# Kernel tuning notes

Hardware: AMD Instinct MI355X
Metric: run time of the kernel (lower is better)

The kernel has to match this reference:

```python
import jax, jax.numpy as jnp
import numpy as np

K_MASK = -2.3819763e+38
B, L, D = 2, 2048, 2048
NQ, NKV, H = 8, 4, 256
Q_SCALE = 0.0625  # head_dim ** -0.5
ROPE_BASE = 10000.0
SOFT_CAP = 50.0
WINDOW = 512
EPS = 1e-6


def apply_rope(x, positions, base=ROPE_BASE):
    # x: [B, L, N, H], positions: [B, L]; rope_proportion=1.0 -> no nope pad
    head_dim = x.shape[-1]
    half = head_dim // 2
    freq_exp = 2.0 / head_dim * jnp.arange(half, dtype=jnp.float32)
    timescale = base ** freq_exp                                   # [H/2]
    ang = positions[..., None].astype(jnp.float32) / timescale     # [B, L, H/2]
    ang = ang[..., None, :]                                        # [B, L, 1, H/2]
    sin, cos = jnp.sin(ang), jnp.cos(ang)
    x1, x2 = jnp.split(x, 2, axis=-1)
    out = jnp.concatenate([x1 * cos - x2 * sin, x2 * cos + x1 * sin], axis=-1)
    return out.astype(x.dtype)


def rms_norm(x, scale, eps=EPS):
    var = jnp.mean(jnp.square(x), axis=-1, keepdims=True)
    return x * jax.lax.rsqrt(var + eps) * (1.0 + scale)


def sliding_window_mask(positions, window):
    # bidirectional window: total size `window` split left/right
    q_pos = positions[:, :, None]
    k_pos = positions[:, None, :]
    dist = q_pos - k_pos
    left = (window + 1) // 2
    right = window // 2 + 1
    return ((dist >= 0) & (dist < left)) | ((dist < 0) & (-dist < right))  # [B, L, L]


def setup_inputs() -> dict:
    key = jax.random.key(0)
    ks = jax.random.split(key, 4)
    x = jax.random.normal(ks[0], (B, L, D), dtype=jnp.float32)
    segment_pos = jnp.tile(jnp.arange(L, dtype=jnp.int32)[None, :], (B, 1))
    attn_mask = jnp.ones((B, L, L), dtype=jnp.bool_)
    q_w = 0.01 * jax.random.normal(ks[1], (NQ, D, H), dtype=jnp.float32)
    kv_w = 0.01 * jax.random.normal(ks[2], (2, NKV, D, H), dtype=jnp.float32)
    o_w = 0.01 * jax.random.normal(ks[3], (NQ, H, D), dtype=jnp.float32)
    q_scale = jnp.zeros((H,), dtype=jnp.float32)
    k_scale = jnp.zeros((H,), dtype=jnp.float32)
    return {"x": x, "segment_pos": segment_pos, "attn_mask": attn_mask,
            "q_w": q_w, "kv_w": kv_w, "o_w": o_w,
            "q_scale": q_scale, "k_scale": k_scale}


def reference(x, segment_pos, attn_mask, q_w, kv_w, o_w, q_scale, k_scale):
    # projections (GQA path: num_kv_heads != num_q_heads)
    q = jnp.einsum('BTD,NDH->BTNH', x, q_w)                   # [B,T,NQ,H]
    kv = jnp.einsum('BSD,CKDH->CBSKH', x, kv_w)
    k, v = kv[0], kv[1]                                       # [B,S,NKV,H]
    # QK-RMSNorm
    q = rms_norm(q, q_scale)
    k = rms_norm(k, k_scale)
    # RoPE + query scaling
    q = apply_rope(q, segment_pos) * Q_SCALE
    k = apply_rope(k, segment_pos)
    # grouped logits
    G = NQ // NKV
    q = q.reshape(B, L, NKV, G, H)
    logits = jnp.einsum('BTKGH,BSKH->BTKGS', q, k).reshape(B, L, NQ, L)
    # soft cap
    logits = jnp.tanh(logits / SOFT_CAP) * SOFT_CAP
    # bidirectional sliding-window mask combined with attn_mask
    mask = attn_mask & sliding_window_mask(segment_pos, WINDOW)  # [B,L,L]
    padded = jnp.where(mask[:, :, None, :], logits, K_MASK)
    probs = jax.nn.softmax(padded, axis=-1).astype(k.dtype)
    probs = probs.reshape(B, L, NKV, G, L)
    enc = jnp.einsum('BTKGS,BSKH->BTKGH', probs, v).reshape(B, L, NQ, H)
    return jnp.einsum('BTNH,NHD->BTD', enc, o_w)
```

## Files before the change

kernel.cpp:

```cpp
#include <hip/hip_runtime.h>
#include <stdint.h>

#define B_   2
#define L_   2048
#define D_   2048
#define NQh  8
#define NKVh 4
#define H_   256

typedef __attribute__((ext_vector_type(8))) short bf16x8;
typedef __attribute__((ext_vector_type(4))) float f32x4;
typedef __attribute__((ext_vector_type(4))) unsigned short u16x4;

typedef __attribute__((address_space(1))) unsigned int as1_uint;
typedef __attribute__((address_space(3))) unsigned int as3_uint;

#define MFMA16(a, b, c) __builtin_amdgcn_mfma_f32_16x16x32_bf16((a), (b), (c), 0, 0, 0)

__device__ __forceinline__ unsigned short f2b(float f) {
  uint32_t u = __builtin_bit_cast(uint32_t, f);
  u += 0x7FFFu + ((u >> 16) & 1u);
  return (unsigned short)(u >> 16);
}

__device__ __forceinline__ void gload16(const unsigned short* g, unsigned short* l) {
  __builtin_amdgcn_global_load_lds((as1_uint*)g, (as3_uint*)l, 16, 0, 0);
}

template<int N> __device__ __forceinline__ void vmwait() {
  if constexpr (N == 8)      asm volatile("s_waitcnt vmcnt(8)" ::: "memory");
  else if constexpr (N == 6) asm volatile("s_waitcnt vmcnt(6)" ::: "memory");
  else if constexpr (N == 4) asm volatile("s_waitcnt vmcnt(4)" ::: "memory");
  else if constexpr (N == 3) asm volatile("s_waitcnt vmcnt(3)" ::: "memory");
  else                       asm volatile("s_waitcnt vmcnt(0)" ::: "memory");
}

__global__ void k_cvt_x(const float* __restrict__ x, unsigned short* __restrict__ xb) {
  int i = blockIdx.x * blockDim.x + threadIdx.x;
  float4 v = ((const float4*)x)[i];
  u16x4 o;
  o.x = f2b(v.x); o.y = f2b(v.y); o.z = f2b(v.z); o.w = f2b(v.w);
  ((u16x4*)xb)[i] = o;
}

__global__ void k_build_wt(const float* __restrict__ qw, const float* __restrict__ kvw,
                           unsigned short* __restrict__ Wt) {
  __shared__ float tile[32][33];
  int hb = blockIdx.z;
  int h0 = blockIdx.y * 32, d0 = blockIdx.x * 32;
  const float* src; int rowbase;
  if (hb < 8) { src = qw + (size_t)hb * D_ * H_;       rowbase = hb * 256; }
  else        { src = kvw + (size_t)(hb - 8) * D_ * H_; rowbase = 2048 + (hb - 8) * 256; }
  int tx = threadIdx.x & 31, ty = threadIdx.x >> 5;
  for (int i = 0; i < 4; i++) {
    int d = ty + i * 8;
    tile[d][tx] = src[(size_t)(d0 + d) * H_ + h0 + tx];
  }
  __syncthreads();
  for (int i = 0; i < 4; i++) {
    int h = ty + i * 8;
    Wt[(size_t)(rowbase + h0 + h) * D_ + d0 + tx] = f2b(tile[tx][h]);
  }
}

__global__ void k_build_owt(const float* __restrict__ ow, unsigned short* __restrict__ Owt) {
  __shared__ float tile[32][33];
  int r0 = blockIdx.y * 32, d0 = blockIdx.x * 32;
  int tx = threadIdx.x & 31, ty = threadIdx.x >> 5;
  for (int i = 0; i < 4; i++) {
    int r = ty + i * 8;
    tile[r][tx] = ow[(size_t)(r0 + r) * D_ + d0 + tx];
  }
  __syncthreads();
  for (int i = 0; i < 4; i++) {
    int d = ty + i * 8;
    Owt[(size_t)(d0 + d) * 2048 + r0 + tx] = f2b(tile[tx][d]);
  }
}

__global__ __launch_bounds__(512, 2) void k_gemm64(const unsigned short* __restrict__ A,
                                                   const unsigned short* __restrict__ Bt,
                                                   float* __restrict__ C, int Ndim, int Kdim) {
  __shared__ __align__(16) unsigned short lds[65536];

  const int t = threadIdx.x;
  const int w = t >> 6, l = t & 63;
  const int wr = w >> 2, wc = w & 3;
  const int g = l >> 4, c = l & 15;
  const int m0 = blockIdx.y * 256, n0 = blockIdx.x * 256;
  const int NI = Kdim >> 7;

  const int chunk = ((l & 3) ^ ((l >> 3) & 3)) * 8;
  const unsigned short* Ag = A  + (size_t)(m0 + w * 16 + (l >> 2)) * Kdim + chunk;
  const unsigned short* Bg = Bt + (size_t)(n0 + w * 16 + (l >> 2)) * Kdim + chunk;
  const int rsw = (g ^ ((c >> 1) & 3)) * 8;

  auto stageA = [&](int kt, int ks) {
    unsigned short* dst = &lds[(kt & 1) * 32768 + ks * 8192 + w * 512];
    const unsigned short* src = Ag + (size_t)kt * 64 + ks * 32;
    gload16(src, dst);
    gload16(src + (size_t)128 * Kdim, dst + 4096);
  };
  auto stageB = [&](int kt, int ks) {
    unsigned short* dst = &lds[(kt & 1) * 32768 + 16384 + ks * 8192 + w * 512];
    const unsigned short* src = Bg + (size_t)kt * 64 + ks * 32;
    gload16(src, dst);
    gload16(src + (size_t)128 * Kdim, dst + 4096);
  };

  bf16x8 af[8];
  auto ldA = [&](int slot, int ks) {
#pragma unroll
    for (int m = 0; m < 8; m++)
      af[m] = *(const bf16x8*)&lds[slot * 32768 + ks * 8192 + (wr * 128 + m * 16 + c) * 32 + rsw];
  };
  auto ldB = [&](int slot, int ks, int n) {
    return *(const bf16x8*)&lds[slot * 32768 + 16384 + ks * 8192 + (wc * 64 + n * 16 + c) * 32 + rsw];
  };

  f32x4 acc[8][4] = {};

#define GPH(SLOT, KS, NH, DO_LDA, STAGE_STMT, VM_STMT)                        \
  {                                                                           \
    if (DO_LDA) ldA(SLOT, KS);                                                \
    bf16x8 b0 = ldB(SLOT, KS, (NH) * 2);                                      \
    bf16x8 b1 = ldB(SLOT, KS, (NH) * 2 + 1);                                  \
    STAGE_STMT;                                                               \
    __builtin_amdgcn_s_barrier();                                             \
    asm volatile("s_waitcnt lgkmcnt(0)" ::: "memory");                        \
    __builtin_amdgcn_s_setprio(1);                                            \
    _Pragma("unroll")                                                         \
    for (int m = 0; m < 8; m++) {                                             \
      acc[m][(NH) * 2]     = MFMA16(af[m], b0, acc[m][(NH) * 2]);             \
      acc[m][(NH) * 2 + 1] = MFMA16(af[m], b1, acc[m][(NH) * 2 + 1]);         \
    }                                                                         \
    __builtin_amdgcn_s_setprio(0);                                            \
    VM_STMT;                                                                  \
    __builtin_amdgcn_s_barrier();                                             \
  }

  stageA(0, 0); stageB(0, 0);
  stageA(0, 1); stageB(0, 1);
  stageA(1, 0); stageB(1, 0);
  vmwait<8>();
  __builtin_amdgcn_s_barrier();

  for (int i = 0; i < NI; i++) {
    const int ta = 2 * i, tb = 2 * i + 1;
    const bool nl = (i + 1 < NI);
    GPH(0, 0, 0, true,  { stageA(tb, 1); }, {});
    GPH(0, 0, 1, false, { stageB(tb, 1); }, { vmwait<8>(); });
    GPH(0, 1, 0, true,  { if (nl) stageA(ta + 2, 0); }, {});
    GPH(0, 1, 1, false, { if (nl) stageB(ta + 2, 0); },
        { if (nl) vmwait<8>(); else vmwait<4>(); });
    GPH(1, 0, 0, true,  { if (nl) stageA(ta + 2, 1); }, {});
    GPH(1, 0, 1, false, { if (nl) stageB(ta + 2, 1); },
        { if (nl) vmwait<8>(); else vmwait<0>(); });
    GPH(1, 1, 0, true,  { if (nl) stageA(tb + 2, 0); }, {});
    GPH(1, 1, 1, false, { if (nl) stageB(tb + 2, 0); }, { if (nl) vmwait<8>(); });
  }
#undef GPH

#pragma unroll
  for (int m = 0; m < 8; m++)
#pragma unroll
    for (int n = 0; n < 4; n++) {
      int row = m0 + wr * 128 + m * 16 + g * 4;
      int col = n0 + wc * 64 + n * 16 + c;
      float* cp = &C[(size_t)row * Ndim + col];
#pragma unroll
      for (int r = 0; r < 4; r++) cp[(size_t)r * Ndim] = acc[m][n][r];
    }
}

template<int BM, int BN>
__global__ __launch_bounds__(512, 2) void k_gemm8p(const unsigned short* __restrict__ A,
                                                   const unsigned short* __restrict__ Bt,
                                                   float* __restrict__ C, int Ndim, int Kdim) {
  constexpr int MF  = BM / 32;
  constexpr int NF  = 4;
  constexpr int ASZ = BM * 32, BSZ = BN * 32;
  constexpr int SLOT = ASZ + BSZ;
  constexpr int LA  = BM / 128, LB = BN / 128;
  constexpr int U   = LA + LB;
  constexpr int NPH = (MF * NF) / 16;
  __shared__ __align__(16) unsigned short lds[4 * SLOT];

  const int t = threadIdx.x;
  const int w = t >> 6, l = t & 63;
  const int wr = w >> 2, wc = w & 3;
  const int g = l >> 4, c = l & 15;
  const int m0 = blockIdx.y * BM, n0 = blockIdx.x * BN;
  const int NT = Kdim >> 5;

  const int kswz = ((l & 3) ^ ((l >> 3) & 3)) * 8;
  const unsigned short* Ag = A  + (size_t)(m0 + w * 16 + (l >> 2)) * Kdim + kswz;
  const unsigned short* Bg = Bt + (size_t)(n0 + w * 16 + (l >> 2)) * Kdim + kswz;
  const int ldsA = w * 512;
  const int ldsB = ASZ + w * 512;
  const int gsw = (g ^ ((c >> 1) & 3)) * 8;

  auto stageA = [&](int kt) {
    int s = kt & 3;
#pragma unroll
    for (int j = 0; j < LA; j++)
      gload16(Ag + (size_t)j * 128 * Kdim + kt * 32, &lds[s * SLOT + ldsA + j * 4096]);
  };
  auto stageB = [&](int kt) {
    int s = kt & 3;
#pragma unroll
    for (int j = 0; j < LB; j++)
      gload16(Bg + (size_t)j * 128 * Kdim + kt * 32, &lds[s * SLOT + ldsB + j * 4096]);
  };

  f32x4 acc[MF][NF] = {};

  stageA(0); stageB(0);
  stageA(1); stageB(1);
  stageA(2); stageB(2);
  vmwait<2 * U>();
  __builtin_amdgcn_s_barrier();

  for (int i = 0; i < NT; i++) {
    const int s = i & 3;
    const unsigned short* As = &lds[s * SLOT];
    const unsigned short* Bs = &lds[s * SLOT + ASZ];
    bf16x8 af[MF];
#pragma unroll
    for (int m = 0; m < MF; m++)
      af[m] = *(const bf16x8*)&As[(wr * (BM / 2) + m * 16 + c) * 32 + gsw];

    if constexpr (NPH == 2) {
      bf16x8 bf0 = *(const bf16x8*)&Bs[(wc * 64 + 0 * 16 + c) * 32 + gsw];
      bf16x8 bf1 = *(const bf16x8*)&Bs[(wc * 64 + 1 * 16 + c) * 32 + gsw];
      if (i + 3 < NT) stageA(i + 3);
      __builtin_amdgcn_s_barrier();
      asm volatile("s_waitcnt lgkmcnt(0)" ::: "memory");
      __builtin_amdgcn_s_setprio(1);
#pragma unroll
      for (int m = 0; m < MF; m++) {
        acc[m][0] = MFMA16(af[m], bf0, acc[m][0]);
        acc[m][1] = MFMA16(af[m], bf1, acc[m][1]);
      }
      __builtin_amdgcn_s_setprio(0);
      __builtin_amdgcn_s_barrier();
      bf16x8 bf2 = *(const bf16x8*)&Bs[(wc * 64 + 2 * 16 + c) * 32 + gsw];
      bf16x8 bf3 = *(const bf16x8*)&Bs[(wc * 64 + 3 * 16 + c) * 32 + gsw];
      if (i + 3 < NT) stageB(i + 3);
      __builtin_amdgcn_s_barrier();
      asm volatile("s_waitcnt lgkmcnt(0)" ::: "memory");
      __builtin_amdgcn_s_setprio(1);
#pragma unroll
      for (int m = 0; m < MF; m++) {
        acc[m][2] = MFMA16(af[m], bf2, acc[m][2]);
        acc[m][3] = MFMA16(af[m], bf3, acc[m][3]);
      }
      __builtin_amdgcn_s_setprio(0);
      if (i < NT - 1) {
        int rem = NT - 2 - i;
        if (rem >= 2)      vmwait<2 * U>();
        else if (rem == 1) vmwait<U>();
        else               vmwait<0>();
      }
      __builtin_amdgcn_s_barrier();
    } else {
      bf16x8 bf[4];
#pragma unroll
      for (int n = 0; n < 4; n++)
        bf[n] = *(const bf16x8*)&Bs[(wc * 64 + n * 16 + c) * 32 + gsw];
      if (i + 3 < NT) { stageA(i + 3); stageB(i + 3); }
      __builtin_amdgcn_s_barrier();
      asm volatile("s_waitcnt lgkmcnt(0)" ::: "memory");
      __builtin_amdgcn_s_setprio(1);
#pragma unroll
      for (int m = 0; m < MF; m++)
#pragma unroll
        for (int n = 0; n < 4; n++)
          acc[m][n] = MFMA16(af[m], bf[n], acc[m][n]);
      __builtin_amdgcn_s_setprio(0);
      if (i < NT - 1) {
        int rem = NT - 2 - i;
        if (rem >= 2)      vmwait<2 * U>();
        else if (rem == 1) vmwait<U>();
        else               vmwait<0>();
      }
      __builtin_amdgcn_s_barrier();
    }
  }

#pragma unroll
  for (int m = 0; m < MF; m++)
#pragma unroll
    for (int n = 0; n < NF; n++) {
      int row = m0 + wr * (BM / 2) + m * 16 + g * 4;
      int col = n0 + wc * 64 + n * 16 + c;
      float* cp = &C[(size_t)row * Ndim + col];
#pragma unroll
      for (int r = 0; r < 4; r++) cp[(size_t)r * Ndim] = acc[m][n][r];
    }
}

__global__ __launch_bounds__(256) void k_postqk(const float* __restrict__ qkv,
    const int* __restrict__ spos, const float* __restrict__ qs, const float* __restrict__ ks,
    unsigned short* __restrict__ qpre, unsigned short* __restrict__ kpre) {
  int wid = blockIdx.x * 4 + (threadIdx.x >> 6);
  int l = threadIdx.x & 63;
  int b, n, tpos, colbase; const float* scl; unsigned short* dst; float qmul;
  if (wid < B_ * NQh * L_) {
    b = wid / (NQh * L_); int rr = wid % (NQh * L_); n = rr / L_; tpos = rr % L_;
    colbase = n * 256; scl = qs; qmul = 0.0625f;
    dst = qpre + ((size_t)(b * NQh + n) * L_ + tpos) * H_;
  } else {
    int r2 = wid - B_ * NQh * L_;
    b = r2 / (NKVh * L_); int rr = r2 % (NKVh * L_); n = rr / L_; tpos = rr % L_;
    colbase = 2048 + n * 256; scl = ks; qmul = 1.0f;
    dst = kpre + ((size_t)(b * NKVh + n) * L_ + tpos) * H_;
  }
  const float4 v = *(const float4*)&qkv[(size_t)(b * L_ + tpos) * 4096 + colbase + l * 4];
  float ss = v.x * v.x + v.y * v.y + v.z * v.z + v.w * v.w;
  for (int m = 1; m < 64; m <<= 1) ss += __shfl_xor(ss, m, 64);
  float inv = rsqrtf(ss * (1.0f / 256.0f) + 1e-6f);
  const float4 sc = *(const float4*)&scl[l * 4];
  float xv[4] = { v.x * inv * (1.f + sc.x), v.y * inv * (1.f + sc.y),
                  v.z * inv * (1.f + sc.z), v.w * inv * (1.f + sc.w) };
  float pf = (float)spos[b * L_ + tpos];
  u16x4 o;
#pragma unroll
  for (int i = 0; i < 4; i++) {
    int h = l * 4 + i, f = h & 127;
    float ts = __expf((float)f * (-9.210340371976184f / 128.0f));
    float ang = pf * ts;
    float s_, c_;
    __sincosf(ang, &s_, &c_);
    float part = __shfl_xor(xv[i], 32, 64);
    float r = (h < 128) ? (xv[i] * c_ - part * s_) : (xv[i] * c_ + part * s_);
    o[i] = f2b(r * qmul);
  }
  *(u16x4*)&dst[l * 4] = o;
}

__global__ void k_vtrans(const float* __restrict__ qkv, unsigned short* __restrict__ vpre) {
  __shared__ float tile[32][33];
  int bz = blockIdx.z; int b = bz >> 2, n = bz & 3;
  int t0 = blockIdx.x * 32, h0 = blockIdx.y * 32;
  int tx = threadIdx.x & 31, ty = threadIdx.x >> 5;
  for (int i = 0; i < 4; i++) {
    int tt = ty + i * 8;
    tile[tt][tx] = qkv[(size_t)(b * L_ + t0 + tt) * 4096 + 3072 + n * H_ + h0 + tx];
  }
  __syncthreads();
  size_t base = ((size_t)(b * NKVh + n) * 64 + (t0 >> 5)) * 8192;
  for (int i = 0; i < 4; i++) {
    int hh = ty + i * 8;
    vpre[base + (size_t)(h0 + hh) * 32 + tx] = f2b(tile[tx][hh]);
  }
}

__global__ __launch_bounds__(256) void k_attn(const unsigned short* __restrict__ qpre,
    const unsigned short* __restrict__ kpre, const unsigned short* __restrict__ vpre,
    unsigned short* __restrict__ enc) {
  __shared__ __align__(16) unsigned short Ksm[32 * 264];
  __shared__ __align__(16) unsigned short Vsm[256 * 40];
  int t = threadIdx.x;
  int wv = t >> 6, l = t & 63;
  int g = l >> 4, c = l & 15;
  int bid = blockIdx.x;
  int qt = bid & 31, n = (bid >> 5) & 7, b = bid >> 8;
  int t0 = qt * 64;
  int kv = n >> 1;
  int q = t0 + wv * 16 + c;

  const unsigned short* qb = qpre + ((size_t)(b * NQh + n) * L_ + t0 + wv * 16 + c) * H_;
  bf16x8 qf[8];
#pragma unroll
  for (int kk = 0; kk < 8; kk++) qf[kk] = *(const bf16x8*)&qb[kk * 32 + g * 8];

  const unsigned short* kh = kpre + (size_t)(b * NKVh + kv) * L_ * H_;
  const unsigned short* vh = vpre + (size_t)(b * NKVh + kv) * 64 * 8192;

  int ksrc = wv * 2048 + l * 8;
  int vsrc = wv * 2048 + l * 8;
  int kdst[4], vdst[4];
#pragma unroll
  for (int j = 0; j < 4; j++) {
    int krow = wv * 8 + j * 2 + (l >> 5);
    kdst[j] = krow * 264 + (l & 31) * 8;
    int vrow = wv * 64 + j * 16 + (l >> 2);
    vdst[j] = vrow * 40 + (l & 3) * 8;
  }

  f32x4 acc[16] = {};
  float lsum = 0.f;

  int c_lo = (t0 >= 256) ? 0 : ((256 - t0) >> 5);
  int c_hi = ((2272 - t0) >> 5) + 1; if (c_hi > 18) c_hi = 18;

  bf16x8 kreg[4], vreg[4];
  {
    int s0 = t0 - 256 + c_lo * 32;
    const unsigned short* kc = kh + (size_t)s0 * 256;
    const unsigned short* vc = vh + (size_t)(s0 >> 5) * 8192;
#pragma unroll
    for (int j = 0; j < 4; j++) {
      kreg[j] = *(const bf16x8*)&kc[ksrc + j * 512];
      vreg[j] = *(const bf16x8*)&vc[vsrc + j * 512];
    }
#pragma unroll
    for (int j = 0; j < 4; j++) {
      *(bf16x8*)&Ksm[kdst[j]] = kreg[j];
      *(bf16x8*)&Vsm[vdst[j]] = vreg[j];
    }
    __syncthreads();
  }

  for (int ci = c_lo; ci < c_hi; ci++) {
    int s0 = t0 - 256 + ci * 32;
    bool have_next = (ci + 1) < c_hi;
    if (have_next) {
      int s1 = s0 + 32;
      const unsigned short* kc = kh + (size_t)s1 * 256;
      const unsigned short* vc = vh + (size_t)(s1 >> 5) * 8192;
#pragma unroll
      for (int j = 0; j < 4; j++) {
        kreg[j] = *(const bf16x8*)&kc[ksrc + j * 512];
        vreg[j] = *(const bf16x8*)&vc[vsrc + j * 512];
      }
    }

    float p[2][4];
#pragma unroll
    for (int half = 0; half < 2; half++) {
      f32x4 st = {};
#pragma unroll
      for (int kk = 0; kk < 8; kk++) {
        bf16x8 kf = *(const bf16x8*)&Ksm[(half * 16 + c) * 264 + kk * 32 + g * 8];
        st = MFMA16(kf, qf[kk], st);
      }
#pragma unroll
      for (int r = 0; r < 4; r++) {
        int key = s0 + half * 16 + g * 4 + r;
        int d = key - q;
        bool valid = (d >= -255) && (d <= 256);
        float e1 = __expf(st[r] * 0.04f);
        float pe = __expf(fmaf(-100.f, __builtin_amdgcn_rcpf(e1 + 1.f), 40.f));
        float pv = valid ? pe : 0.f;
        p[half][r] = pv;
        lsum += pv;
      }
    }

    uint32_t pk[4];
#pragma unroll
    for (int r = 0; r < 4; r++)
      pk[r] = (uint32_t)f2b(p[0][r]) | ((uint32_t)f2b(p[1][r]) << 16);
    uint32_t rv[2][4];
#pragma unroll
    for (int jj = 0; jj < 2; jj++) {
      int srcl = (((l >> 4) & 1) * 2 + jj) * 16 + c;
#pragma unroll
      for (int r = 0; r < 4; r++)
        rv[jj][r] = (uint32_t)__shfl((int)pk[r], srcl, 64);
    }
    union { uint32_t u[4]; bf16x8 v8; } pb;
    int hi = g >> 1;
#pragma unroll
    for (int p2 = 0; p2 < 4; p2++) {
      uint32_t w0 = rv[p2 >> 1][(2 * p2) & 3];
      uint32_t w1 = rv[p2 >> 1][((2 * p2) & 3) + 1];
      uint32_t e0 = hi ? (w0 >> 16) : (w0 & 0xFFFFu);
      uint32_t e1 = hi ? (w1 >> 16) : (w1 & 0xFFFFu);
      pb.u[p2] = e0 | (e1 << 16);
    }
#pragma unroll
    for (int ht = 0; ht < 16; ht++) {
      bf16x8 vf = *(const bf16x8*)&Vsm[(ht * 16 + c) * 40 + g * 8];
      acc[ht] = MFMA16(vf, pb.v8, acc[ht]);
    }

    __syncthreads();
    if (have_next) {
#pragma unroll
      for (int j = 0; j < 4; j++) {
        *(bf16x8*)&Ksm[kdst[j]] = kreg[j];
        *(bf16x8*)&Vsm[vdst[j]] = vreg[j];
      }
    }
    __syncthreads();
  }

  lsum += __shfl_xor(lsum, 16, 64);
  lsum += __shfl_xor(lsum, 32, 64);
  float invl = 1.0f / lsum;
  unsigned short* eb = enc + ((size_t)(b * L_ + t0 + wv * 16 + c)) * 2048 + n * 256;
#pragma unroll
  for (int ht = 0; ht < 16; ht++) {
    u16x4 o;
#pragma unroll
    for (int r = 0; r < 4; r++) o[r] = f2b(acc[ht][r] * invl);
    *(u16x4*)&eb[ht * 16 + g * 4] = o;
  }
}

extern "C" void kernel_launch(void* const* d_in, const int* in_sizes, int n_in,
                              void* d_out, int out_size, void* d_ws, size_t ws_size,
                              hipStream_t stream) {
  const float* x   = (const float*)d_in[0];
  const int* spos  = (const int*)d_in[1];
  const float* qw  = (const float*)d_in[3];
  const float* kvw = (const float*)d_in[4];
  const float* ow  = (const float*)d_in[5];
  const float* qs  = (const float*)d_in[6];
  const float* ks  = (const float*)d_in[7];
  float* out = (float*)d_out;

  char* p = (char*)d_ws;
  unsigned short* xb   = (unsigned short*)p; p += (size_t)4096 * 2048 * 2;
  unsigned short* Wt   = (unsigned short*)p; p += (size_t)4096 * 2048 * 2;
  unsigned short* Owt  = (unsigned short*)p; p += (size_t)2048 * 2048 * 2;
  float*          qkv  = (float*)p;          p += (size_t)4096 * 4096 * 4;
  unsigned short* qpre = (unsigned short*)p; p += (size_t)B_ * NQh * L_ * H_ * 2;
  unsigned short* kpre = (unsigned short*)p; p += (size_t)B_ * NKVh * L_ * H_ * 2;
  unsigned short* vpre = (unsigned short*)p; p += (size_t)B_ * NKVh * L_ * H_ * 2;
  unsigned short* enc  = (unsigned short*)p; p += (size_t)4096 * 2048 * 2;

  k_cvt_x<<<8192, 256, 0, stream>>>(x, xb);
  k_build_wt<<<dim3(64, 8, 16), 256, 0, stream>>>(qw, kvw, Wt);
  k_build_owt<<<dim3(64, 64), 256, 0, stream>>>(ow, Owt);
  k_gemm64<<<dim3(16, 16), 512, 0, stream>>>(xb, Wt, qkv, 4096, 2048);
  k_postqk<<<12288, 256, 0, stream>>>(qkv, spos, qs, ks, qpre, kpre);
  k_vtrans<<<dim3(64, 8, 8), 256, 0, stream>>>(qkv, vpre);
  k_attn<<<512, 256, 0, stream>>>(qpre, kpre, vpre, enc);
  k_gemm8p<128, 256><<<dim3(8, 32), 512, 0, stream>>>(enc, Owt, out, 2048, 2048);
}
```

Before: 198.7 us.

## Store QKV projection in bf16, double-buffer attention K/V tiles, add MFMA priority hints

The QKV GEMM now writes bf16 instead of fp32, which halves the intermediate buffer traffic for the GEMM epilogue and for the post-QK and V-transpose kernels that read it. The V-transpose kernel is rewritten to use vectorized 4-element bf16 loads and stores. The attention kernel double-buffers its K/V shared-memory tiles so one barrier per iteration is removed, and it wraps the MFMA loops in s_setprio hints. Rounding q/k/v to bf16 before the RMS norm adds some precision loss, and the double buffer doubles LDS use, which may reduce occupancy.

```diff
diff --git a/kernel.cpp b/kernel.cpp
--- a/kernel.cpp
+++ b/kernel.cpp
@@ -21,6 +21,10 @@
   uint32_t u = __builtin_bit_cast(uint32_t, f);
   u += 0x7FFFu + ((u >> 16) & 1u);
   return (unsigned short)(u >> 16);
+}
+__device__ __forceinline__ float b2f(unsigned short s) {
+  uint32_t u = (uint32_t)s << 16;
+  return __builtin_bit_cast(float, u);
 }
 
 __device__ __forceinline__ void gload16(const unsigned short* g, unsigned short* l) {
@@ -80,7 +84,8 @@
 
 __global__ __launch_bounds__(512, 2) void k_gemm64(const unsigned short* __restrict__ A,
                                                    const unsigned short* __restrict__ Bt,
-                                                   float* __restrict__ C, int Ndim, int Kdim) {
+                                                   unsigned short* __restrict__ C,
+                                                   int Ndim, int Kdim) {
   __shared__ __align__(16) unsigned short lds[65536];
 
   const int t = threadIdx.x;
@@ -167,9 +172,9 @@
     for (int n = 0; n < 4; n++) {
       int row = m0 + wr * 128 + m * 16 + g * 4;
       int col = n0 + wc * 64 + n * 16 + c;
-      float* cp = &C[(size_t)row * Ndim + col];
-#pragma unroll
-      for (int r = 0; r < 4; r++) cp[(size_t)r * Ndim] = acc[m][n][r];
+      unsigned short* cp = &C[(size_t)row * Ndim + col];
+#pragma unroll
+      for (int r = 0; r < 4; r++) cp[(size_t)r * Ndim] = f2b(acc[m][n][r]);
     }
 }
 
@@ -300,7 +305,7 @@
     }
 }
 
-__global__ __launch_bounds__(256) void k_postqk(const float* __restrict__ qkv,
+__global__ __launch_bounds__(256) void k_postqk(const unsigned short* __restrict__ qkvb,
     const int* __restrict__ spos, const float* __restrict__ qs, const float* __restrict__ ks,
     unsigned short* __restrict__ qpre, unsigned short* __restrict__ kpre) {
   int wid = blockIdx.x * 4 + (threadIdx.x >> 6);
@@ -316,13 +321,14 @@
     colbase = 2048 + n * 256; scl = ks; qmul = 1.0f;
     dst = kpre + ((size_t)(b * NKVh + n) * L_ + tpos) * H_;
   }
-  const float4 v = *(const float4*)&qkv[(size_t)(b * L_ + tpos) * 4096 + colbase + l * 4];
-  float ss = v.x * v.x + v.y * v.y + v.z * v.z + v.w * v.w;
+  const u16x4 v4 = *(const u16x4*)&qkvb[(size_t)(b * L_ + tpos) * 4096 + colbase + l * 4];
+  float vv[4] = { b2f(v4.x), b2f(v4.y), b2f(v4.z), b2f(v4.w) };
+  float ss = vv[0] * vv[0] + vv[1] * vv[1] + vv[2] * vv[2] + vv[3] * vv[3];
   for (int m = 1; m < 64; m <<= 1) ss += __shfl_xor(ss, m, 64);
   float inv = rsqrtf(ss * (1.0f / 256.0f) + 1e-6f);
   const float4 sc = *(const float4*)&scl[l * 4];
-  float xv[4] = { v.x * inv * (1.f + sc.x), v.y * inv * (1.f + sc.y),
-                  v.z * inv * (1.f + sc.z), v.w * inv * (1.f + sc.w) };
+  float xv[4] = { vv[0] * inv * (1.f + sc.x), vv[1] * inv * (1.f + sc.y),
+                  vv[2] * inv * (1.f + sc.z), vv[3] * inv * (1.f + sc.w) };
   float pf = (float)spos[b * L_ + tpos];
   u16x4 o;
 #pragma unroll
@@ -339,28 +345,31 @@
   *(u16x4*)&dst[l * 4] = o;
 }
 
-__global__ void k_vtrans(const float* __restrict__ qkv, unsigned short* __restrict__ vpre) {
-  __shared__ float tile[32][33];
+__global__ void k_vtrans(const unsigned short* __restrict__ qkvb,
+                         unsigned short* __restrict__ vpre) {
+  __shared__ unsigned short tile[32][36];
   int bz = blockIdx.z; int b = bz >> 2, n = bz & 3;
   int t0 = blockIdx.x * 32, h0 = blockIdx.y * 32;
-  int tx = threadIdx.x & 31, ty = threadIdx.x >> 5;
-  for (int i = 0; i < 4; i++) {
-    int tt = ty + i * 8;
-    tile[tt][tx] = qkv[(size_t)(b * L_ + t0 + tt) * 4096 + 3072 + n * H_ + h0 + tx];
-  }
+  int ty = threadIdx.x >> 3;
+  int tx4 = (threadIdx.x & 7) * 4;
+  *(u16x4*)&tile[ty][tx4] =
+      *(const u16x4*)&qkvb[(size_t)(b * L_ + t0 + ty) * 4096 + 3072 + n * H_ + h0 + tx4];
   __syncthreads();
   size_t base = ((size_t)(b * NKVh + n) * 64 + (t0 >> 5)) * 8192;
-  for (int i = 0; i < 4; i++) {
-    int hh = ty + i * 8;
-    vpre[base + (size_t)(h0 + hh) * 32 + tx] = f2b(tile[tx][hh]);
-  }
+  int hh = threadIdx.x >> 3;
+  int tw4 = (threadIdx.x & 7) * 4;
+  u16x4 o;
+#pragma unroll
+  for (int j = 0; j < 4; j++) o[j] = tile[tw4 + j][hh];
+  *(u16x4*)&vpre[base + (size_t)(h0 + hh) * 32 + tw4] = o;
 }
 
 __global__ __launch_bounds__(256) void k_attn(const unsigned short* __restrict__ qpre,
     const unsigned short* __restrict__ kpre, const unsigned short* __restrict__ vpre,
     unsigned short* __restrict__ enc) {
-  __shared__ __align__(16) unsigned short Ksm[32 * 264];
-  __shared__ __align__(16) unsigned short Vsm[256 * 40];
+  constexpr int KSZ = 32 * 264, VSZ = 256 * 40;
+  __shared__ __align__(16) unsigned short Ksm[2 * KSZ];
+  __shared__ __align__(16) unsigned short Vsm[2 * VSZ];
   int t = threadIdx.x;
   int wv = t >> 6, l = t & 63;
   int g = l >> 4, c = l & 15;
@@ -400,6 +409,7 @@
     int s0 = t0 - 256 + c_lo * 32;
     const unsigned short* kc = kh + (size_t)s0 * 256;
     const unsigned short* vc = vh + (size_t)(s0 >> 5) * 8192;
+    int sl = c_lo & 1;
 #pragma unroll
     for (int j = 0; j < 4; j++) {
       kreg[j] = *(const bf16x8*)&kc[ksrc + j * 512];
@@ -407,14 +417,15 @@
     }
 #pragma unroll
     for (int j = 0; j < 4; j++) {
-      *(bf16x8*)&Ksm[kdst[j]] = kreg[j];
-      *(bf16x8*)&Vsm[vdst[j]] = vreg[j];
+      *(bf16x8*)&Ksm[sl * KSZ + kdst[j]] = kreg[j];
+      *(bf16x8*)&Vsm[sl * VSZ + vdst[j]] = vreg[j];
     }
     __syncthreads();
   }
 
   for (int ci = c_lo; ci < c_hi; ci++) {
     int s0 = t0 - 256 + ci * 32;
+    int sl = ci & 1;
     bool have_next = (ci + 1) < c_hi;
     if (have_next) {
       int s1 = s0 + 32;
@@ -431,11 +442,13 @@
 #pragma unroll
     for (int half = 0; half < 2; half++) {
       f32x4 st = {};
+      __builtin_amdgcn_s_setprio(1);
 #pragma unroll
       for (int kk = 0; kk < 8; kk++) {
-        bf16x8 kf = *(const bf16x8*)&Ksm[(half * 16 + c) * 264 + kk * 32 + g * 8];
+        bf16x8 kf = *(const bf16x8*)&Ksm[sl * KSZ + (half * 16 + c) * 264 + kk * 32 + g * 8];
         st = MFMA16(kf, qf[kk], st);
       }
+      __builtin_amdgcn_s_setprio(0);
 #pragma unroll
       for (int r = 0; r < 4; r++) {
         int key = s0 + half * 16 + g * 4 + r;
@@ -471,18 +484,20 @@
       uint32_t e1 = hi ? (w1 >> 16) : (w1 & 0xFFFFu);
       pb.u[p2] = e0 | (e1 << 16);
     }
+    __builtin_amdgcn_s_setprio(1);
 #pragma unroll
     for (int ht = 0; ht < 16; ht++) {
-      bf16x8 vf = *(const bf16x8*)&Vsm[(ht * 16 + c) * 40 + g * 8];
+      bf16x8 vf = *(const bf16x8*)&Vsm[sl * VSZ + (ht * 16 + c) * 40 + g * 8];
       acc[ht] = MFMA16(vf, pb.v8, acc[ht]);
     }
-
-    __syncthreads();
+    __builtin_amdgcn_s_setprio(0);
+
     if (have_next) {
+      int s2 = sl ^ 1;
 #pragma unroll
       for (int j = 0; j < 4; j++) {
-        *(bf16x8*)&Ksm[kdst[j]] = kreg[j];
-        *(bf16x8*)&Vsm[vdst[j]] = vreg[j];
+        *(bf16x8*)&Ksm[s2 * KSZ + kdst[j]] = kreg[j];
+        *(bf16x8*)&Vsm[s2 * VSZ + vdst[j]] = vreg[j];
       }
     }
     __syncthreads();
@@ -517,7 +532,7 @@
   unsigned short* xb   = (unsigned short*)p; p += (size_t)4096 * 2048 * 2;
   unsigned short* Wt   = (unsigned short*)p; p += (size_t)4096 * 2048 * 2;
   unsigned short* Owt  = (unsigned short*)p; p += (size_t)2048 * 2048 * 2;
-  float*          qkv  = (float*)p;          p += (size_t)4096 * 4096 * 4;
+  unsigned short* qkvb = (unsigned short*)p; p += (size_t)4096 * 4096 * 2;
   unsigned short* qpre = (unsigned short*)p; p += (size_t)B_ * NQh * L_ * H_ * 2;
   unsigned short* kpre = (unsigned short*)p; p += (size_t)B_ * NKVh * L_ * H_ * 2;
   unsigned short* vpre = (unsigned short*)p; p += (size_t)B_ * NKVh * L_ * H_ * 2;
@@ -526,9 +541,9 @@
   k_cvt_x<<<8192, 256, 0, stream>>>(x, xb);
   k_build_wt<<<dim3(64, 8, 16), 256, 0, stream>>>(qw, kvw, Wt);
   k_build_owt<<<dim3(64, 64), 256, 0, stream>>>(ow, Owt);
-  k_gemm64<<<dim3(16, 16), 512, 0, stream>>>(xb, Wt, qkv, 4096, 2048);
-  k_postqk<<<12288, 256, 0, stream>>>(qkv, spos, qs, ks, qpre, kpre);
-  k_vtrans<<<dim3(64, 8, 8), 256, 0, stream>>>(qkv, vpre);
+  k_gemm64<<<dim3(16, 16), 512, 0, stream>>>(xb, Wt, qkvb, 4096, 2048);
+  k_postqk<<<12288, 256, 0, stream>>>(qkvb, spos, qs, ks, qpre, kpre);
+  k_vtrans<<<dim3(64, 8, 8), 256, 0, stream>>>(qkvb, vpre);
   k_attn<<<512, 256, 0, stream>>>(qpre, kpre, vpre, enc);
   k_gemm8p<128, 256><<<dim3(8, 32), 512, 0, stream>>>(enc, Owt, out, 2048, 2048);
 }
```

New measurement: 192.9 us. 1.03x faster.
